# Optimization experiments

Hardware: AMD Instinct MI355X
Metric: run time of the kernel (lower is better)

The kernel has to match this reference:

```python
import jax, jax.numpy as jnp
import numpy as np

B, S, DM = 1, 2048, 1024
H, D, T = 16, 64, 16
NA = 3  # anchor tiles per query (local tile appended -> 4 tiles, 64 tokens)


def setup_inputs() -> dict:
    key = jax.random.key(0)
    ks = jax.random.split(key, 6)
    sc = 1.0 / np.sqrt(DM)
    x = jax.random.normal(ks[0], (B, S, DM), jnp.float32)
    Wq = jax.random.normal(ks[1], (DM, H * D), jnp.float32) * sc
    Wk = jax.random.normal(ks[2], (DM, H * D), jnp.float32) * sc
    Wv = jax.random.normal(ks[3], (DM, H * D), jnp.float32) * sc
    Wo = jax.random.normal(ks[4], (H * D, DM), jnp.float32) * sc
    anchor_indices = jax.random.randint(ks[5], (B, H, S, NA), 0, S // T).astype(jnp.int32)
    # RoPE freqs: freqs_cis[s, j] = exp(i * s * theta_j), half-split convention
    half = D // 2
    inv_freq = 1.0 / (10000.0 ** (np.arange(half, dtype=np.float64) / half))
    ang = np.outer(np.arange(S), inv_freq)  # [S, half]
    cos = jnp.asarray(np.cos(ang), jnp.float32)
    sin = jnp.asarray(np.sin(ang), jnp.float32)
    return {"x": x, "Wq": Wq, "Wk": Wk, "Wv": Wv, "Wo": Wo,
            "cos": cos, "sin": sin, "anchor_indices": anchor_indices}


def _rotate_half(z):
    h = z.shape[-1] // 2
    return jnp.concatenate([-z[..., h:], z[..., :h]], axis=-1)


def reference(x, Wq, Wk, Wv, Wo, cos, sin, anchor_indices):
    b, s, _ = x.shape
    # projections -> [B, H, S, D]
    q = (x @ Wq).reshape(b, s, H, D).transpose(0, 2, 1, 3)
    k = (x @ Wk).reshape(b, s, H, D).transpose(0, 2, 1, 3)
    v = (x @ Wv).reshape(b, s, H, D).transpose(0, 2, 1, 3)
    # RoPE (half-split / rotate_half)
    cos_f = jnp.concatenate([cos, cos], axis=-1)[None, None]  # [1,1,S,D]
    sin_f = jnp.concatenate([sin, sin], axis=-1)[None, None]
    q = q * cos_f + _rotate_half(q) * sin_f
    k = k * cos_f + _rotate_half(k) * sin_f
    # tile index set: anchor tiles + local tile
    local = (jnp.arange(s) // T).astype(jnp.int32)
    local = jnp.broadcast_to(local[None, None, :, None], (b, H, s, 1))
    tiles = jnp.concatenate([anchor_indices, local], axis=-1)  # [B,H,S,NA+1]
    tok = tiles[..., None] * T + jnp.arange(T, dtype=jnp.int32)  # [B,H,S,NA+1,T]
    K = (NA + 1) * T  # sparse_len
    idx = jnp.clip(tok.reshape(b, H, s, K), 0, s - 1)
    # per-(b,h) per-query gather of K/V -> [B,H,S,K,D]
    gather = jax.vmap(jax.vmap(lambda kv, i: kv[i]))
    k_sp = gather(k, idx)
    v_sp = gather(v, idx)
    logits = jnp.einsum('bhqd,bhqkd->bhqk', q, k_sp) / jnp.sqrt(jnp.float32(D))
    qidx = jnp.arange(s)[None, None, :, None]
    fut = idx > qidx  # causal mask over gathered keys
    logits = jnp.where(fut, -1e10, logits)
    w = jax.nn.softmax(logits, axis=-1)
    fully_masked = jnp.all(fut, axis=-1, keepdims=True)
    w = jnp.where(fully_masked, 0.0, w)
    w = jnp.where(jnp.isnan(w), 0.0, w)
    out = jnp.einsum('bhqk,bhqkd->bhqd', w, v_sp)
    out = out.transpose(0, 2, 1, 3).reshape(b, s, H * D)
    return out @ Wo
```

## Files before the change

### kernel.cpp

```cpp
#include <hip/hip_runtime.h>
#include <hip/hip_bf16.h>


#define S_LEN 2048
#define DM 1024
#define NH 16
#define HD 64

typedef __bf16 bf16x8 __attribute__((ext_vector_type(8)));
typedef float f32x4 __attribute__((ext_vector_type(4)));

static __device__ __forceinline__ unsigned short f2bf(float f) {
    union { float f; unsigned int i; } un;
    un.f = f;
    unsigned int r = un.i + 0x7FFFu + ((un.i >> 16) & 1u);
    return (unsigned short)(r >> 16);
}
static __device__ __forceinline__ float bfu2f(unsigned short u) {
    union { unsigned int i; float f; } un;
    un.i = ((unsigned int)u) << 16;
    return un.f;
}
static __device__ __forceinline__ float bflo(unsigned int u) {
    union { unsigned int i; float f; } un;
    un.i = u << 16;
    return un.f;
}
static __device__ __forceinline__ float bfhi(unsigned int u) {
    union { unsigned int i; float f; } un;
    un.i = u & 0xFFFF0000u;
    return un.f;
}

static __device__ __forceinline__ void gll16(const unsigned short* g,
                                             unsigned short* l) {
    __builtin_amdgcn_global_load_lds(
        (const __attribute__((address_space(1))) unsigned int*)(uintptr_t)g,
        (__attribute__((address_space(3))) unsigned int*)(uintptr_t)l,
        16, 0, 0);
}

__global__ __launch_bounds__(256) void prep(
    const float* __restrict__ x, unsigned short* __restrict__ xb,
    const float* __restrict__ W0, const float* __restrict__ W1,
    const float* __restrict__ W2, const float* __restrict__ W3,
    unsigned short* __restrict__ T0, unsigned short* __restrict__ T1,
    unsigned short* __restrict__ T2, unsigned short* __restrict__ T3) {
    const int bx = blockIdx.x;
    if (bx < 1024) {
        const int z = bx >> 8, rem = bx & 255;
        const float* W = (z == 0) ? W0 : (z == 1) ? W1 : (z == 2) ? W2 : W3;
        unsigned short* T = (z == 0) ? T0 : (z == 1) ? T1 : (z == 2) ? T2 : T3;
        __shared__ float t[64][65];
        const int bn = (rem & 15) * 64, bk = (rem >> 4) * 64;
        const int tx = threadIdx.x & 63, ty = threadIdx.x >> 6;
        #pragma unroll
        for (int m = 0; m < 16; ++m)
            t[ty + m * 4][tx] = W[(size_t)(bk + ty + m * 4) * 1024 + bn + tx];
        __syncthreads();
        #pragma unroll
        for (int m = 0; m < 16; ++m)
            T[(size_t)(bn + ty + m * 4) * 1024 + bk + tx] =
                f2bf(t[tx][ty + m * 4]);
    } else {
        const int i = (bx - 1024) * 2048 + threadIdx.x * 8;
        float4 f0 = *(const float4*)(x + i);
        float4 f1 = *(const float4*)(x + i + 4);
        ushort4 o0, o1;
        o0.x = f2bf(f0.x); o0.y = f2bf(f0.y); o0.z = f2bf(f0.z); o0.w = f2bf(f0.w);
        o1.x = f2bf(f1.x); o1.y = f2bf(f1.y); o1.z = f2bf(f1.z); o1.w = f2bf(f1.w);
        *(ushort4*)(xb + i) = o0;
        *(ushort4*)(xb + i + 4) = o1;
    }
}

__global__ __launch_bounds__(256) void gemm_qkv(
    const unsigned short* __restrict__ xb,
    const unsigned short* __restrict__ Wtq, const unsigned short* __restrict__ Wtk,
    const unsigned short* __restrict__ Wtv,
    unsigned short* __restrict__ qh, unsigned short* __restrict__ kh,
    unsigned short* __restrict__ vh,
    const float* __restrict__ cs, const float* __restrict__ sn) {
    __shared__ __align__(16) unsigned short Al[2][64 * 32];
    __shared__ __align__(16) unsigned short Bl[2][128 * 32];
    const int tid = threadIdx.x;
    const int nb = blockIdx.x >> 3;
    const unsigned short* __restrict__ Bt = (nb == 0) ? Wtq : (nb == 1) ? Wtk : Wtv;
    unsigned short* __restrict__ OUT = (nb == 0) ? qh : (nb == 1) ? kh : vh;
    const int col0 = (blockIdx.x & 7) * 128;
    const int row0 = blockIdx.y * 64;
    const int lane = tid & 63, wvi = tid >> 6;
    const int wr = (wvi >> 1) * 32, wc = (wvi & 1) * 64;
    const int l15 = lane & 15, quad = lane >> 4;

    const int grow = lane >> 2;
    const int gkc = (lane & 3) * 8;
    const unsigned short* gA = xb + (size_t)(row0 + wvi * 16 + grow) * 1024 + gkc;
    const unsigned short* gB = Bt + (size_t)(col0 + wvi * 32 + grow) * 1024 + gkc;
    const int lAo = (wvi * 16) * 32;
    const int lBo = (wvi * 32) * 32;

    f32x4 acc[2][4] = {};
    gll16(gA, Al[0] + lAo);
    gll16(gB, Bl[0] + lBo);
    gll16(gB + 16 * 1024, Bl[0] + lBo + 16 * 32);
    __syncthreads();
    for (int it = 0; it < 32; ++it) {
        const int cur = it & 1;
        if (it < 31) {
            const int k1 = (it + 1) * 32;
            gll16(gA + k1, Al[cur ^ 1] + lAo);
            gll16(gB + k1, Bl[cur ^ 1] + lBo);
            gll16(gB + 16 * 1024 + k1, Bl[cur ^ 1] + lBo + 16 * 32);
        }
        bf16x8 af[2], bfr[4];
        #pragma unroll
        for (int i = 0; i < 2; ++i)
            af[i] = *(const bf16x8*)&Al[cur][(wr + i * 16 + l15) * 32 + quad * 8];
        #pragma unroll
        for (int j = 0; j < 4; ++j)
            bfr[j] = *(const bf16x8*)&Bl[cur][(wc + j * 16 + l15) * 32 + quad * 8];
        #pragma unroll
        for (int i = 0; i < 2; ++i)
            #pragma unroll
            for (int j = 0; j < 4; ++j)
                acc[i][j] = __builtin_amdgcn_mfma_f32_16x16x32_bf16(
                    af[i], bfr[j], acc[i][j], 0, 0, 0);
        __syncthreads();
    }

    const int hh = ((blockIdx.x & 7) << 1) + (wc >> 6);
    const bool dorope = (nb != 2);
    #pragma unroll
    for (int i = 0; i < 2; ++i) {
        const int rowb = row0 + wr + i * 16 + quad * 4;
        #pragma unroll
        for (int r = 0; r < 4; ++r) {
            const int s = rowb + r;
            float v0 = acc[i][0][r], v1 = acc[i][1][r];
            float v2 = acc[i][2][r], v3 = acc[i][3][r];
            if (dorope) {
                float c0 = cs[s * 32 + l15],      s0 = sn[s * 32 + l15];
                float c1 = cs[s * 32 + 16 + l15], s1 = sn[s * 32 + 16 + l15];
                float lo0 = v0 * c0 - v2 * s0;
                float hi0 = v2 * c0 + v0 * s0;
                float lo1 = v1 * c1 - v3 * s1;
                float hi1 = v3 * c1 + v1 * s1;
                v0 = lo0; v1 = lo1; v2 = hi0; v3 = hi1;
            }
            unsigned short* op = OUT + (size_t)hh * (S_LEN * 64) + (size_t)s * 64 + l15;
            op[0]  = f2bf(v0);
            op[16] = f2bf(v1);
            op[32] = f2bf(v2);
            op[48] = f2bf(v3);
        }
    }
}

__global__ __launch_bounds__(256) void attn_kernel(
    const unsigned short* __restrict__ qh, const unsigned short* __restrict__ kh,
    const unsigned short* __restrict__ vh, const int* __restrict__ anc,
    unsigned short* __restrict__ att) {
    __shared__ __align__(16) float qs[4][64];
    __shared__ __align__(16) int   ts[4][64];
    __shared__ __align__(16) float ws[4][64];
    const int w4 = threadIdx.x >> 6;
    const int lane = threadIdx.x & 63;
    const int bid = blockIdx.x;
    const int xcd = bid & 7;
    const int idx = bid >> 3;
    const int h   = (xcd << 1) | (idx >> 9);
    const int qi  = ((idx & 511) << 2) + w4;
    const size_t hb = (size_t)h * (S_LEN * 64);

    const float q_own = bfu2f(qh[hb + (size_t)qi * 64 + lane]);
    const int slot = lane >> 4;
    const int tile = (slot < 3) ? anc[((size_t)h * S_LEN + qi) * 3 + slot]
                                : (qi >> 4);
    const int tok_own = tile * 16 + (lane & 15);
    qs[w4][lane] = q_own;
    ts[w4][lane] = tok_own;

    const int c = lane & 3;
    const int t = lane >> 2;
    float qv[16];
    #pragma unroll
    for (int r = 0; r < 4; ++r) {
        float4 f = *(const float4*)&qs[w4][c * 16 + r * 4];
        qv[r * 4 + 0] = f.x; qv[r * 4 + 1] = f.y;
        qv[r * 4 + 2] = f.z; qv[r * 4 + 3] = f.w;
    }

    #pragma unroll
    for (int p = 0; p < 4; ++p) {
        const int tk = ts[w4][p * 16 + t];
        const unsigned short* kp = kh + hb + (size_t)tk * 64 + c * 16;
        const uint4 k0 = *(const uint4*)kp;
        const uint4 k1 = *(const uint4*)(kp + 8);
        float part;
        part = bflo(k0.x) * qv[0];
        part = fmaf(bfhi(k0.x), qv[1], part);
        part = fmaf(bflo(k0.y), qv[2], part);
        part = fmaf(bfhi(k0.y), qv[3], part);
        part = fmaf(bflo(k0.z), qv[4], part);
        part = fmaf(bfhi(k0.z), qv[5], part);
        part = fmaf(bflo(k0.w), qv[6], part);
        part = fmaf(bfhi(k0.w), qv[7], part);
        part = fmaf(bflo(k1.x), qv[8], part);
        part = fmaf(bfhi(k1.x), qv[9], part);
        part = fmaf(bflo(k1.y), qv[10], part);
        part = fmaf(bfhi(k1.y), qv[11], part);
        part = fmaf(bflo(k1.z), qv[12], part);
        part = fmaf(bfhi(k1.z), qv[13], part);
        part = fmaf(bflo(k1.w), qv[14], part);
        part = fmaf(bfhi(k1.w), qv[15], part);
        part += __shfl_xor(part, 1, 64);
        part += __shfl_xor(part, 2, 64);
        if (c == 0) ws[w4][p * 16 + t] = part;
    }

    float logit = ws[w4][lane];
    const bool fut = tok_own > qi;
    logit = fut ? -1e30f : logit * 0.125f;

    float m = logit;
    #pragma unroll
    for (int off = 32; off >= 1; off >>= 1)
        m = fmaxf(m, __shfl_xor(m, off, 64));
    const float e = fut ? 0.f : __expf(logit - m);
    float ssum = e;
    #pragma unroll
    for (int off = 32; off >= 1; off >>= 1)
        ssum += __shfl_xor(ssum, off, 64);
    ws[w4][lane] = e / ssum;

    const int tq = lane >> 4;
    const int dd = lane & 15;
    const unsigned short* vbase = vh + hb + dd * 4;
    float a0 = 0.f, a1 = 0.f, a2 = 0.f, a3 = 0.f;
    #pragma unroll
    for (int r = 0; r < 16; ++r) {
        const int kk = r * 4 + tq;
        const int tok = ts[w4][kk];
        const uint2 vv = *(const uint2*)(vbase + (size_t)tok * 64);
        const float w = ws[w4][kk];
        a0 = fmaf(w, bflo(vv.x), a0);
        a1 = fmaf(w, bfhi(vv.x), a1);
        a2 = fmaf(w, bflo(vv.y), a2);
        a3 = fmaf(w, bfhi(vv.y), a3);
    }
    a0 += __shfl_xor(a0, 16, 64); a0 += __shfl_xor(a0, 32, 64);
    a1 += __shfl_xor(a1, 16, 64); a1 += __shfl_xor(a1, 32, 64);
    a2 += __shfl_xor(a2, 16, 64); a2 += __shfl_xor(a2, 32, 64);
    a3 += __shfl_xor(a3, 16, 64); a3 += __shfl_xor(a3, 32, 64);
    if (tq == 0) {
        ushort4 o;
        o.x = f2bf(a0); o.y = f2bf(a1); o.z = f2bf(a2); o.w = f2bf(a3);
        *(ushort4*)&att[(size_t)qi * DM + h * HD + dd * 4] = o;
    }
}

__global__ __launch_bounds__(256) void gemm_out(
    const unsigned short* __restrict__ A, const unsigned short* __restrict__ Bt,
    float* __restrict__ C) {
    __shared__ __align__(16) unsigned short Al[2][64 * 32];
    __shared__ __align__(16) unsigned short Bl[2][64 * 32];
    const int tid = threadIdx.x;
    const int col0 = blockIdx.x * 64;
    const int row0 = blockIdx.y * 64;
    const int lane = tid & 63, wvi = tid >> 6;
    const int wr = (wvi >> 1) * 32, wc = (wvi & 1) * 32;
    const int l15 = lane & 15, quad = lane >> 4;

    const int grow = lane >> 2;
    const int gkc = (lane & 3) * 8;
    const unsigned short* gA = A + (size_t)(row0 + wvi * 16 + grow) * 1024 + gkc;
    const unsigned short* gB = Bt + (size_t)(col0 + wvi * 16 + grow) * 1024 + gkc;
    const int lAo = (wvi * 16) * 32;
    const int lBo = (wvi * 16) * 32;

    f32x4 acc[2][2] = {};
    gll16(gA, Al[0] + lAo);
    gll16(gB, Bl[0] + lBo);
    __syncthreads();
    for (int it = 0; it < 32; ++it) {
        const int cur = it & 1;
        if (it < 31) {
            const int k1 = (it + 1) * 32;
            gll16(gA + k1, Al[cur ^ 1] + lAo);
            gll16(gB + k1, Bl[cur ^ 1] + lBo);
        }
        bf16x8 af[2], bfr[2];
        #pragma unroll
        for (int i = 0; i < 2; ++i)
            af[i] = *(const bf16x8*)&Al[cur][(wr + i * 16 + l15) * 32 + quad * 8];
        #pragma unroll
        for (int j = 0; j < 2; ++j)
            bfr[j] = *(const bf16x8*)&Bl[cur][(wc + j * 16 + l15) * 32 + quad * 8];
        #pragma unroll
        for (int i = 0; i < 2; ++i)
            #pragma unroll
            for (int j = 0; j < 2; ++j)
                acc[i][j] = __builtin_amdgcn_mfma_f32_16x16x32_bf16(
                    af[i], bfr[j], acc[i][j], 0, 0, 0);
        __syncthreads();
    }
    #pragma unroll
    for (int i = 0; i < 2; ++i) {
        const int rowb = row0 + wr + i * 16 + quad * 4;
        #pragma unroll
        for (int r = 0; r < 4; ++r) {
            float* crow = C + (size_t)(rowb + r) * 1024 + col0 + wc;
            #pragma unroll
            for (int j = 0; j < 2; ++j)
                crow[j * 16 + l15] = acc[i][j][r];
        }
    }
}

extern "C" void kernel_launch(void* const* d_in, const int* in_sizes, int n_in,
                              void* d_out, int out_size, void* d_ws, size_t ws_size,
                              hipStream_t stream) {
    const float* x   = (const float*)d_in[0];
    const float* Wq  = (const float*)d_in[1];
    const float* Wk  = (const float*)d_in[2];
    const float* Wv  = (const float*)d_in[3];
    const float* Wo  = (const float*)d_in[4];
    const float* cs  = (const float*)d_in[5];
    const float* sn  = (const float*)d_in[6];
    const int*   anc = (const int*)d_in[7];
    float* out = (float*)d_out;

    unsigned short* xb  = (unsigned short*)d_ws;
    unsigned short* Wtq = xb  + (size_t)2048 * 1024;
    unsigned short* Wtk = Wtq + (size_t)1024 * 1024;
    unsigned short* Wtv = Wtk + (size_t)1024 * 1024;
    unsigned short* Wto = Wtv + (size_t)1024 * 1024;
    unsigned short* qh  = Wto + (size_t)1024 * 1024;
    unsigned short* kh  = qh  + (size_t)2048 * 1024;
    unsigned short* vh  = kh  + (size_t)2048 * 1024;
    unsigned short* att = vh  + (size_t)2048 * 1024;

    prep<<<2048, 256, 0, stream>>>(x, xb, Wq, Wk, Wv, Wo, Wtq, Wtk, Wtv, Wto);
    gemm_qkv<<<dim3(24, 32), 256, 0, stream>>>(xb, Wtq, Wtk, Wtv,
                                               qh, kh, vh, cs, sn);
    attn_kernel<<<(S_LEN * NH) / 4, 256, 0, stream>>>(qh, kh, vh, anc, att);
    gemm_out<<<dim3(16, 32), 256, 0, stream>>>(att, Wto, out);
}
```

Baseline: 146.5 us.

## Triple-buffer LDS with prefetch distance two in QKV and output GEMMs

Measured after the change: 145.4 us. No clear change (-0.8%).

```diff
diff --git a/kernel.cpp b/kernel.cpp
--- a/kernel.cpp
+++ b/kernel.cpp
@@ -81,8 +81,8 @@
     unsigned short* __restrict__ qh, unsigned short* __restrict__ kh,
     unsigned short* __restrict__ vh,
     const float* __restrict__ cs, const float* __restrict__ sn) {
-    __shared__ __align__(16) unsigned short Al[2][64 * 32];
-    __shared__ __align__(16) unsigned short Bl[2][128 * 32];
+    __shared__ __align__(16) unsigned short Al[3][64 * 32];
+    __shared__ __align__(16) unsigned short Bl[3][128 * 32];
     const int tid = threadIdx.x;
     const int nb = blockIdx.x >> 3;
     const unsigned short* __restrict__ Bt = (nb == 0) ? Wtq : (nb == 1) ? Wtk : Wtv;
@@ -104,15 +104,13 @@
     gll16(gA, Al[0] + lAo);
     gll16(gB, Bl[0] + lBo);
     gll16(gB + 16 * 1024, Bl[0] + lBo + 16 * 32);
-    __syncthreads();
+    gll16(gA + 32, Al[1] + lAo);
+    gll16(gB + 32, Bl[1] + lBo);
+    gll16(gB + 16 * 1024 + 32, Bl[1] + lBo + 16 * 32);
+    asm volatile("s_waitcnt vmcnt(3)" ::: "memory");
+    __builtin_amdgcn_s_barrier();
+    int cur = 0;
     for (int it = 0; it < 32; ++it) {
-        const int cur = it & 1;
-        if (it < 31) {
-            const int k1 = (it + 1) * 32;
-            gll16(gA + k1, Al[cur ^ 1] + lAo);
-            gll16(gB + k1, Bl[cur ^ 1] + lBo);
-            gll16(gB + 16 * 1024 + k1, Bl[cur ^ 1] + lBo + 16 * 32);
-        }
         bf16x8 af[2], bfr[4];
         #pragma unroll
         for (int i = 0; i < 2; ++i)
@@ -120,13 +118,25 @@
         #pragma unroll
         for (int j = 0; j < 4; ++j)
             bfr[j] = *(const bf16x8*)&Bl[cur][(wc + j * 16 + l15) * 32 + quad * 8];
+        if (it < 30) {
+            const int k2 = (it + 2) * 32;
+            const int st = (cur + 2 >= 3) ? cur - 1 : cur + 2;
+            gll16(gA + k2, Al[st] + lAo);
+            gll16(gB + k2, Bl[st] + lBo);
+            gll16(gB + 16 * 1024 + k2, Bl[st] + lBo + 16 * 32);
+        }
         #pragma unroll
         for (int i = 0; i < 2; ++i)
             #pragma unroll
             for (int j = 0; j < 4; ++j)
                 acc[i][j] = __builtin_amdgcn_mfma_f32_16x16x32_bf16(
                     af[i], bfr[j], acc[i][j], 0, 0, 0);
-        __syncthreads();
+        if (it < 30)
+            asm volatile("s_waitcnt vmcnt(3)" ::: "memory");
+        else
+            asm volatile("s_waitcnt vmcnt(0)" ::: "memory");
+        __builtin_amdgcn_s_barrier();
+        cur = (cur >= 2) ? 0 : cur + 1;
     }
 
     const int hh = ((blockIdx.x & 7) << 1) + (wc >> 6);
@@ -263,8 +273,8 @@
 __global__ __launch_bounds__(256) void gemm_out(
     const unsigned short* __restrict__ A, const unsigned short* __restrict__ Bt,
     float* __restrict__ C) {
-    __shared__ __align__(16) unsigned short Al[2][64 * 32];
-    __shared__ __align__(16) unsigned short Bl[2][64 * 32];
+    __shared__ __align__(16) unsigned short Al[3][64 * 32];
+    __shared__ __align__(16) unsigned short Bl[3][64 * 32];
     const int tid = threadIdx.x;
     const int col0 = blockIdx.x * 64;
     const int row0 = blockIdx.y * 64;
@@ -282,14 +292,12 @@
     f32x4 acc[2][2] = {};
     gll16(gA, Al[0] + lAo);
     gll16(gB, Bl[0] + lBo);
-    __syncthreads();
+    gll16(gA + 32, Al[1] + lAo);
+    gll16(gB + 32, Bl[1] + lBo);
+    asm volatile("s_waitcnt vmcnt(2)" ::: "memory");
+    __builtin_amdgcn_s_barrier();
+    int cur = 0;
     for (int it = 0; it < 32; ++it) {
-        const int cur = it & 1;
-        if (it < 31) {
-            const int k1 = (it + 1) * 32;
-            gll16(gA + k1, Al[cur ^ 1] + lAo);
-            gll16(gB + k1, Bl[cur ^ 1] + lBo);
-        }
         bf16x8 af[2], bfr[2];
         #pragma unroll
         for (int i = 0; i < 2; ++i)
@@ -297,13 +305,24 @@
         #pragma unroll
         for (int j = 0; j < 2; ++j)
             bfr[j] = *(const bf16x8*)&Bl[cur][(wc + j * 16 + l15) * 32 + quad * 8];
+        if (it < 30) {
+            const int k2 = (it + 2) * 32;
+            const int st = (cur + 2 >= 3) ? cur - 1 : cur + 2;
+            gll16(gA + k2, Al[st] + lAo);
+            gll16(gB + k2, Bl[st] + lBo);
+        }
         #pragma unroll
         for (int i = 0; i < 2; ++i)
             #pragma unroll
             for (int j = 0; j < 2; ++j)
                 acc[i][j] = __builtin_amdgcn_mfma_f32_16x16x32_bf16(
                     af[i], bfr[j], acc[i][j], 0, 0, 0);
-        __syncthreads();
+        if (it < 30)
+            asm volatile("s_waitcnt vmcnt(2)" ::: "memory");
+        else
+            asm volatile("s_waitcnt vmcnt(0)" ::: "memory");
+        __builtin_amdgcn_s_barrier();
+        cur = (cur >= 2) ? 0 : cur + 1;
     }
     #pragma unroll
     for (int i = 0; i < 2; ++i) {
```
